# Kernel optimization log

Hardware: AMD Instinct MI355X
Metric: run time of the kernel (lower is better)

Reference implementation:

```python
import jax, jax.numpy as jnp
import numpy as np

NUM_Q_HEADS = 32
NUM_KV_HEADS = 8
HEAD_DIM = 128
ROPE_THETA = 10000.0


def _apply_rope(x, positions):
    # x: (B, T, H, D) real; rotate pairs (x[2i], x[2i+1]) by angle pos * inv_freq[i]
    B, T, H, D = x.shape
    half = D // 2
    inv_freq = 1.0 / (ROPE_THETA ** (jnp.arange(half, dtype=jnp.float32) / half))
    freqs = positions.astype(jnp.float32)[:, None] * inv_freq[None, :]  # (T, half)
    cos = jnp.cos(freqs)[None, :, None, :]  # (1, T, 1, half)
    sin = jnp.sin(freqs)[None, :, None, :]
    xr = x.reshape(B, T, H, half, 2)
    x1, x2 = xr[..., 0], xr[..., 1]
    o1 = x1 * cos - x2 * sin
    o2 = x1 * sin + x2 * cos
    return jnp.stack([o1, o2], axis=-1).reshape(B, T, H, D)


def setup_inputs() -> dict:
    key = jax.random.key(0)
    ks = jax.random.split(key, 8)
    B, T, C = 2, 1024, 4096
    x = jax.random.normal(ks[0], (B, T, C), dtype=jnp.float32)
    cache_keys = jax.random.normal(ks[1], (B, 4096, NUM_KV_HEADS, HEAD_DIM), dtype=jnp.float32)
    cache_values = jax.random.normal(ks[2], (B, 4096, NUM_KV_HEADS, HEAD_DIM), dtype=jnp.float32)
    s = 0.02
    Wq = jax.random.normal(ks[3], (C, C), dtype=jnp.float32) * s
    Wk = jax.random.normal(ks[4], (NUM_KV_HEADS * HEAD_DIM, C), dtype=jnp.float32) * s
    Wv = jax.random.normal(ks[5], (NUM_KV_HEADS * HEAD_DIM, C), dtype=jnp.float32) * s
    Wo = jax.random.normal(ks[6], (C, C), dtype=jnp.float32) * s
    return {"x": x, "start_pos": 1024, "cache_keys": cache_keys,
            "cache_values": cache_values, "Wq": Wq, "Wk": Wk, "Wv": Wv, "Wo": Wo}


def reference(x, start_pos, cache_keys, cache_values, Wq, Wk, Wv, Wo):
    B, T, C = x.shape
    D = HEAD_DIM
    G = NUM_Q_HEADS // NUM_KV_HEADS  # queries per kv head
    end_pos = start_pos + T
    scale = 1.0 / np.sqrt(D).astype(np.float32)

    # QKV projections (torch Linear: y = x @ W.T)
    q = jnp.einsum('btc,oc->bto', x, Wq).reshape(B, T, NUM_Q_HEADS, D)
    k = jnp.einsum('btc,oc->bto', x, Wk).reshape(B, T, NUM_KV_HEADS, D)
    v = jnp.einsum('btc,oc->bto', x, Wv).reshape(B, T, NUM_KV_HEADS, D)

    # RoPE at absolute positions [start_pos, end_pos)
    positions = jnp.arange(start_pos, end_pos)
    q = _apply_rope(q, positions)
    k = _apply_rope(k, positions)

    # KV-cache write (detached in the original -> stop_gradient)
    cache_keys = cache_keys.at[:, start_pos:end_pos].set(jax.lax.stop_gradient(k))
    cache_values = cache_values.at[:, start_pos:end_pos].set(jax.lax.stop_gradient(v))
    k_full = jax.lax.stop_gradient(cache_keys[:, :end_pos])   # (B, S, Hkv, D)
    v_full = jax.lax.stop_gradient(cache_values[:, :end_pos])
    S = end_pos

    # GQA attention without materializing repeated K/V:
    # q heads h map to kv head h // G (repeat_interleave ordering)
    qg = q.reshape(B, T, NUM_KV_HEADS, G, D)
    scores = jnp.einsum('btkgd,bskd->bkgts', qg, k_full) * scale  # (B,Hkv,G,T,S)

    # causal mask over the cache: query i sees cache positions j <= start_pos + i
    i = jnp.arange(T)[:, None]
    j = jnp.arange(S)[None, :]
    visible = j <= (start_pos + i)  # (T, S)
    scores = jnp.where(visible[None, None, None], scores, jnp.finfo(scores.dtype).min)
    probs = jax.nn.softmax(scores, axis=-1)

    ctx = jnp.einsum('bkgts,bskd->btkgd', probs, v_full).reshape(B, T, C)
    return jnp.einsum('btc,oc->bto', ctx, Wo)
```

## Files before the change

kernel.cpp:

```cpp
#include <hip/hip_runtime.h>
#include <math.h>


typedef __bf16 bf16x8 __attribute__((ext_vector_type(8)));
typedef float floatx4 __attribute__((ext_vector_type(4)));
typedef float floatx16 __attribute__((ext_vector_type(16)));

constexpr int SMAX = 2048;
constexpr size_t KT_OFF = (size_t)2 * 1024 * 4096;
constexpr size_t VT_OFF = KT_OFF + (size_t)2 * 8 * SMAX * 128;
constexpr size_t WS_XB = 0;
constexpr size_t WS_WQ = 8388608;
constexpr size_t WS_WK = 25165824;
constexpr size_t WS_WV = 29360128;
constexpr size_t WS_WO = 33554432;
constexpr size_t WS_FULL_BYTES = 100663296;

__device__ __forceinline__ unsigned short f2bf(float f) {
  union { float f; unsigned int u; } v; v.f = f;
  unsigned int u = v.u;
  return (unsigned short)((u + 0x7fffu + ((u >> 16) & 1u)) >> 16);
}

__device__ __forceinline__ bf16x8 pack8(float4 a, float4 b) {
  bf16x8 v;
  v[0] = (__bf16)a.x; v[1] = (__bf16)a.y; v[2] = (__bf16)a.z; v[3] = (__bf16)a.w;
  v[4] = (__bf16)b.x; v[5] = (__bf16)b.y; v[6] = (__bf16)b.z; v[7] = (__bf16)b.w;
  return v;
}

__device__ __forceinline__ unsigned cvtpk_bf16(float lo, float hi) {
  unsigned r;
  asm("v_cvt_pk_bf16_f32 %0, %1, %2" : "=v"(r) : "v"(lo), "v"(hi));
  return r;
}

__device__ __forceinline__ void gll16(const unsigned short* g, unsigned short* l) {
  __builtin_amdgcn_global_load_lds((const __attribute__((address_space(1))) void*)g,
                                   (__attribute__((address_space(3))) void*)l, 16, 0, 0);
}

__global__ __launch_bounds__(256) void cvt_x(const float* __restrict__ x,
                                             unsigned short* __restrict__ xb) {
  for (size_t c = (size_t)blockIdx.x * 256 + threadIdx.x; c < 1048576; c += (size_t)gridDim.x * 256) {
    float4 f0 = ((const float4*)x)[c * 2], f1 = ((const float4*)x)[c * 2 + 1];
    ((bf16x8*)xb)[c] = pack8(f0, f1);
  }
}

__global__ __launch_bounds__(256) void cvt_full(const float* __restrict__ x,
                                                const float* __restrict__ wq,
                                                const float* __restrict__ wk,
                                                const float* __restrict__ wv,
                                                const float* __restrict__ wo,
                                                unsigned short* __restrict__ ws) {
  const size_t n0 = 1048576, n1 = n0 + 2097152, n2 = n1 + 524288, n3 = n2 + 524288, n4 = n3 + 2097152;
  for (size_t c = (size_t)blockIdx.x * 256 + threadIdx.x; c < n4; c += (size_t)gridDim.x * 256) {
    const float* src; unsigned short* dst; size_t off;
    if (c < n0)      { src = x;  dst = ws + WS_XB; off = c; }
    else if (c < n1) { src = wq; dst = ws + WS_WQ; off = c - n0; }
    else if (c < n2) { src = wk; dst = ws + WS_WK; off = c - n1; }
    else if (c < n3) { src = wv; dst = ws + WS_WV; off = c - n2; }
    else             { src = wo; dst = ws + WS_WO; off = c - n3; }
    float4 f0 = ((const float4*)src)[off * 2], f1 = ((const float4*)src)[off * 2 + 1];
    ((bf16x8*)dst)[off] = pack8(f0, f1);
  }
}

__global__ __launch_bounds__(256) void rope_prep(const int* __restrict__ spp,
                                                 float* __restrict__ tab) {
  int idx = blockIdx.x * 256 + threadIdx.x;
  int t = idx >> 6, i = idx & 63;
  float ang = (float)(spp[0] + t) * exp2f(-(float)i * 0.2076205059304602f);
  tab[idx] = sinf(ang);
  tab[65536 + idx] = cosf(ang);
}

__global__ __launch_bounds__(256) void convert_cache(const float* __restrict__ ck,
                                                     const float* __restrict__ cv,
                                                     const int* __restrict__ spp,
                                                     unsigned short* __restrict__ kt,
                                                     unsigned short* __restrict__ vt) {
  const int sp = spp[0];
  const int bk = blockIdx.y;
  const int b = bk >> 3, kh = bk & 7;
  const int s1 = blockIdx.x * 128;
  if (s1 >= sp) return;
  const int tid = threadIdx.x;
#pragma unroll
  for (int it = 0; it < 8; ++it) {
    int c = tid + it * 256;
    int s = c >> 4, dc = (c & 15) * 8;
    if (s1 + s < sp) {
      const float* src = ck + (((size_t)(b * 4096 + s1 + s)) * 8 + kh) * 128 + dc;
      *(bf16x8*)(kt + ((size_t)bk * SMAX + s1 + s) * 128 + dc) = pack8(*(const float4*)src, *(const float4*)(src + 4));
    }
  }
#pragma unroll
  for (int it = 0; it < 8; ++it) {
    int c = tid + it * 256;
    int d = c & 127, sg = c >> 7;
    bf16x8 tmp;
#pragma unroll
    for (int ss = 0; ss < 8; ++ss) {
      int s = s1 + sg * 8 + ss;
      tmp[ss] = (s < sp) ? (__bf16)cv[(((size_t)(b * 4096 + s)) * 8 + kh) * 128 + d] : (__bf16)0.0f;
    }
    *(bf16x8*)(vt + (size_t)bk * 128 * SMAX + (size_t)d * SMAX + s1 + sg * 8) = tmp;
  }
}

template<bool BDMA, int EPI>
__global__ __launch_bounds__(256) void gemm_core(const unsigned short* __restrict__ A,
                                                 const unsigned short* __restrict__ Bb,
                                                 const float* __restrict__ Bq,
                                                 const float* __restrict__ Bk,
                                                 const float* __restrict__ Bv,
                                                 float* __restrict__ Cout,
                                                 unsigned short* __restrict__ qb,
                                                 unsigned short* __restrict__ kt,
                                                 unsigned short* __restrict__ vt,
                                                 const float* __restrict__ tab,
                                                 const int* __restrict__ spp) {
  constexpr int SB = BDMA ? 32 : 40;
  __shared__ __align__(16) unsigned short la[128 * 32];
  __shared__ __align__(16) unsigned short lb[128 * SB];
  const int K = 4096;
  const int tid = threadIdx.x, lane = tid & 63, wv = tid >> 6;
  const int quad = lane >> 4, l16 = lane & 15;
  const int wm = (wv >> 1) * 64, wn = (wv & 1) * 64;
  const int m0 = blockIdx.y * 128, n0 = blockIdx.x * 128;
  const int sp = spp ? spp[0] : 0;

  floatx4 acc[4][4] = {};

  const int r0 = tid >> 2, kc0 = (tid & 3) * 8;
  const int r1 = (tid + 256) >> 2, kc1 = ((tid + 256) & 3) * 8;
  const unsigned short* a0 = A + (size_t)(m0 + r0) * K + kc0;
  const unsigned short* a1 = A + (size_t)(m0 + r1) * K + kc1;

  const unsigned short* bh0 = nullptr; const unsigned short* bh1 = nullptr;
  const float* bf0 = nullptr; const float* bf1 = nullptr;
  if (BDMA) {
    bh0 = Bb + (size_t)(n0 + r0) * K + kc0;
    bh1 = Bb + (size_t)(n0 + r1) * K + kc1;
  } else {
    const float* Bf; int nb;
    if (EPI == 0)      { Bf = Bq; nb = n0; }
    else {
      if (n0 < 4096)      { Bf = Bq; nb = n0; }
      else if (n0 < 5120) { Bf = Bk; nb = n0 - 4096; }
      else                { Bf = Bv; nb = n0 - 5120; }
    }
    bf0 = Bf + (size_t)(nb + r0) * K + kc0;
    bf1 = Bf + (size_t)(nb + r1) * K + kc1;
  }

  for (int k0 = 0; k0 < K; k0 += 32) {
    gll16(a0 + k0, la + tid * 8);
    gll16(a1 + k0, la + (tid + 256) * 8);
    if (BDMA) {
      gll16(bh0 + k0, lb + tid * 8);
      gll16(bh1 + k0, lb + (tid + 256) * 8);
    } else {
      bf16x8 vb0 = pack8(*(const float4*)(bf0 + k0), *(const float4*)(bf0 + k0 + 4));
      bf16x8 vb1 = pack8(*(const float4*)(bf1 + k0), *(const float4*)(bf1 + k0 + 4));
      *(bf16x8*)(lb + r0 * 40 + kc0) = vb0;
      *(bf16x8*)(lb + r1 * 40 + kc1) = vb1;
    }
    __syncthreads();
    bf16x8 af[4], bfr[4];
#pragma unroll
    for (int mi = 0; mi < 4; ++mi)
      af[mi] = *(const bf16x8*)(la + (wm + mi * 16 + l16) * 32 + quad * 8);
#pragma unroll
    for (int ni = 0; ni < 4; ++ni)
      bfr[ni] = *(const bf16x8*)(lb + (wn + ni * 16 + l16) * SB + quad * 8);
#pragma unroll
    for (int mi = 0; mi < 4; ++mi)
#pragma unroll
      for (int ni = 0; ni < 4; ++ni)
        acc[mi][ni] = __builtin_amdgcn_mfma_f32_16x16x32_bf16(af[mi], bfr[ni], acc[mi][ni], 0, 0, 0);
    __syncthreads();
  }

  if (EPI == 0) {
#pragma unroll
    for (int mi = 0; mi < 4; ++mi)
#pragma unroll
      for (int r = 0; r < 4; ++r) {
        const int row = m0 + wm + mi * 16 + quad * 4 + r;
#pragma unroll
        for (int ni = 0; ni < 4; ++ni)
          Cout[(size_t)row * 4096 + n0 + wn + ni * 16 + l16] = acc[mi][ni][r];
      }
  } else {
    const float S_L2E = 0.12751745f;
#pragma unroll
    for (int mi = 0; mi < 4; ++mi) {
#pragma unroll
      for (int r = 0; r < 4; ++r) {
        const int row = m0 + wm + mi * 16 + quad * 4 + r;
        const int b = row >> 10, t = row & 1023;
#pragma unroll
        for (int ni = 0; ni < 4; ++ni) {
          const int col = n0 + wn + ni * 16 + l16;
          float v = acc[mi][ni][r];
          if (col < 5120) {
            int dd = col & 127, i = dd >> 1;
            float sn = tab[t * 64 + i], cs = tab[65536 + t * 64 + i];
            float vp = __shfl_xor(v, 1, 64);
            float o = (dd & 1) ? (vp * sn + v * cs) : (v * cs - vp * sn);
            if (col < 4096) {
              qb[(size_t)row * 4096 + col] = f2bf(o * S_L2E);
            } else {
              int lc = col - 4096, kh = lc >> 7, d = lc & 127;
              kt[((size_t)(b * 8 + kh) * SMAX + sp + t) * 128 + d] = f2bf(o);
            }
          } else {
            int lc = col - 5120, kh = lc >> 7, d = lc & 127;
            vt[((size_t)(b * 8 + kh) * 128 + d) * SMAX + sp + t] = f2bf(v);
          }
        }
      }
    }
  }
}

__global__ __launch_bounds__(512, 2) void attn(const unsigned short* __restrict__ qb,
                                               const unsigned short* __restrict__ ktg,
                                               const unsigned short* __restrict__ vtg,
                                               const int* __restrict__ spp,
                                               unsigned short* __restrict__ ctx) {
  __shared__ __align__(16) unsigned short lds[32768];

  const int sp = spp[0];
  const int iblk = (int)blockIdx.y * 4 + (int)blockIdx.x;
  const int lblk = (iblk & 7) * 32 + (iblk >> 3);
  const int x = lblk & 3, bh = lblk >> 2;
  const int b = bh >> 5, h = bh & 31;
  const int bk = b * 8 + (h >> 2);
  const int tid = threadIdx.x, lane = tid & 63, w = tid >> 6;
  const int hi = lane >> 5, l31 = lane & 31;
  const int tq128 = (w < 4) ? x : (7 - x);
  const int wq0 = tq128 * 128 + (w & 3) * 32;
  const int q = wq0 + l31;
  const int lim = sp + q;
  const int wlim = sp + wq0 + 31;
  const int nt = (sp + (8 - x) * 128 + 63) >> 6;

  const unsigned short* ktb = ktg + (size_t)bk * SMAX * 128;
  const unsigned short* vtb = vtg + (size_t)bk * 128 * SMAX;

  const int kr0 = tid >> 4, kc = tid & 15, kr1 = kr0 + 32;
  const int ksl0 = ((kc ^ (kr0 & 15)) << 3), ksl1 = ((kc ^ (kr1 & 15)) << 3);
  const int vd0 = tid >> 3, vc = tid & 7, vd1 = vd0 + 64;
  const int vsl0 = ((vc ^ (vd0 & 7)) << 3), vsl1 = ((vc ^ (vd1 & 7)) << 3);

  bf16x8 qf[8];
  {
    const unsigned short* qbase = qb + ((size_t)(b * 1024 + q)) * 4096 + h * 128 + hi * 8;
#pragma unroll
    for (int kg = 0; kg < 8; ++kg) qf[kg] = *(const bf16x8*)(qbase + kg * 16);
  }

  floatx16 oacc[4] = {};
  float mrun = -1e30f, lrun = 0.0f;

  *(bf16x8*)(lds + kr0 * 128 + ksl0)         = *(const bf16x8*)(ktb + (size_t)kr0 * 128 + kc * 8);
  *(bf16x8*)(lds + kr1 * 128 + ksl1)         = *(const bf16x8*)(ktb + (size_t)kr1 * 128 + kc * 8);
  *(bf16x8*)(lds + 16384 + vd0 * 64 + vsl0)  = *(const bf16x8*)(vtb + (size_t)vd0 * SMAX + vc * 8);
  *(bf16x8*)(lds + 16384 + vd1 * 64 + vsl1)  = *(const bf16x8*)(vtb + (size_t)vd1 * SMAX + vc * 8);
  __syncthreads();

  int off = 0;
  for (int st = 0; st < nt; ++st) {
    const int s0 = st * 64;
    bf16x8 nk0, nk1, nv0, nv1;
    const bool pre = (st + 1 < nt);
    if (pre) {
      const int s1 = s0 + 64;
      nk0 = *(const bf16x8*)(ktb + (size_t)(s1 + kr0) * 128 + kc * 8);
      nk1 = *(const bf16x8*)(ktb + (size_t)(s1 + kr1) * 128 + kc * 8);
      nv0 = *(const bf16x8*)(vtb + (size_t)vd0 * SMAX + s1 + vc * 8);
      nv1 = *(const bf16x8*)(vtb + (size_t)vd1 * SMAX + s1 + vc * 8);
      asm volatile("" ::: "memory");
    }
    const unsigned short* kl = lds + off;
    const unsigned short* vl = lds + 16384 + off;
    if (s0 <= wlim) {
#pragma unroll
      for (int sub = 0; sub < 2; ++sub) {
        const int ss = s0 + sub * 32;
        if (ss <= wlim) {
          floatx16 sa = {0,0,0,0,0,0,0,0,0,0,0,0,0,0,0,0};
          const unsigned short* kbase = kl + (sub * 32 + l31) * 128;
          const int kx = l31 & 15;
#pragma unroll
          for (int kg = 0; kg < 8; ++kg) {
            bf16x8 kf = *(const bf16x8*)(kbase + (((kg * 2 + hi) ^ kx) << 3));
            sa = __builtin_amdgcn_mfma_f32_32x32x16_bf16(kf, qf[kg], sa, 0, 0, 0);
          }
          if (ss + 31 > sp + wq0) {
#pragma unroll
            for (int r = 0; r < 16; ++r) {
              const int j = ss + (r & 3) + 8 * (r >> 2) + 4 * hi;
              if (j > lim) sa[r] = -1e30f;
            }
          }
          float mt = sa[0];
#pragma unroll
          for (int r = 1; r < 16; ++r) mt = fmaxf(mt, sa[r]);
          mt = fmaxf(mt, __shfl_xor(mt, 32, 64));
          if (!__all(mt <= mrun + 8.0f)) {
            const float mnew = fmaxf(mrun, mt);
            const float al = exp2f(mrun - mnew);
#pragma unroll
            for (int db = 0; db < 4; ++db)
#pragma unroll
              for (int r = 0; r < 16; ++r) oacc[db][r] *= al;
            lrun *= al;
            mrun = mnew;
          }
          float p[16]; float ls = 0.0f;
#pragma unroll
          for (int r = 0; r < 16; ++r) { p[r] = exp2f(sa[r] - mrun); ls += p[r]; }
          lrun += ls + __shfl_xor(ls, 32, 64);
#pragma unroll
          for (int ks = 0; ks < 2; ++ks) {
            const int rb = ks * 8;
            unsigned a0 = cvtpk_bf16(p[rb + 0], p[rb + 1]);
            unsigned a1 = cvtpk_bf16(p[rb + 2], p[rb + 3]);
            unsigned b0 = cvtpk_bf16(p[rb + 4], p[rb + 5]);
            unsigned b1 = cvtpk_bf16(p[rb + 6], p[rb + 7]);
            const unsigned t0 = __shfl_xor(a0, 32, 64);
            const unsigned t1 = __shfl_xor(b0, 32, 64);
            const unsigned t2 = __shfl_xor(a1, 32, 64);
            const unsigned t3 = __shfl_xor(b1, 32, 64);
            union { unsigned u[4]; bf16x8 v; } pf;
            pf.u[0] = hi ? t1 : a0;
            pf.u[1] = hi ? t3 : a1;
            pf.u[2] = hi ? b0 : t0;
            pf.u[3] = hi ? b1 : t2;
            const int sslot = sub * 4 + ks * 2 + hi;
#pragma unroll
            for (int db = 0; db < 4; ++db) {
              const int vrow = db * 32 + l31;
              bf16x8 vf = *(const bf16x8*)(vl + vrow * 64 + ((sslot ^ (l31 & 7)) << 3));
              oacc[db] = __builtin_amdgcn_mfma_f32_32x32x16_bf16(vf, pf.v, oacc[db], 0, 0, 0);
            }
          }
        }
      }
    }
    if (pre) {
      unsigned short* kn = lds + (off ^ 8192);
      unsigned short* vn = lds + 16384 + (off ^ 8192);
      *(bf16x8*)(kn + kr0 * 128 + ksl0) = nk0;
      *(bf16x8*)(kn + kr1 * 128 + ksl1) = nk1;
      *(bf16x8*)(vn + vd0 * 64 + vsl0) = nv0;
      *(bf16x8*)(vn + vd1 * 64 + vsl1) = nv1;
    }
    __syncthreads();
    off ^= 8192;
  }

  const float invl = 1.0f / lrun;
  unsigned short* myo = lds + w * 4096;
#pragma unroll
  for (int db = 0; db < 4; ++db)
#pragma unroll
    for (int i2 = 0; i2 < 8; ++i2) {
      const int r = i2 * 2;
      const int d = db * 32 + (r & 3) + 8 * (r >> 2) + 4 * hi;
      const unsigned wo = cvtpk_bf16(oacc[db][r] * invl, oacc[db][r + 1] * invl);
      *(unsigned*)(myo + l31 * 128 + (((2 * d) ^ ((l31 & 15) << 4)) >> 1)) = wo;
    }
  __syncthreads();
#pragma unroll
  for (int it = 0; it < 8; ++it) {
    const int c = tid + it * 512;
    const int wr = c >> 9, row = (c >> 4) & 31, c16 = c & 15;
    const int tq = (((wr < 4) ? x : (7 - x)) * 128) + (wr & 3) * 32 + row;
    bf16x8 vv = *(const bf16x8*)(lds + wr * 4096 + row * 128 + ((c16 ^ (row & 15)) << 3));
    *(bf16x8*)(ctx + ((size_t)(b * 1024 + tq)) * 4096 + h * 128 + c16 * 8) = vv;
  }
}

extern "C" void kernel_launch(void* const* d_in, const int* in_sizes, int n_in,
                              void* d_out, int out_size, void* d_ws, size_t ws_size,
                              hipStream_t stream) {
  const float* x  = (const float*)d_in[0];
  const int* sp   = (const int*)d_in[1];
  float* ck       = (float*)d_in[2];
  const float* cv = (const float*)d_in[3];
  const float* Wq = (const float*)d_in[4];
  const float* Wk = (const float*)d_in[5];
  const float* Wv = (const float*)d_in[6];
  const float* Wo = (const float*)d_in[7];
  float* out      = (float*)d_out;

  unsigned short* qb  = (unsigned short*)d_out;
  unsigned short* kt  = (unsigned short*)d_out + KT_OFF;
  unsigned short* vt  = (unsigned short*)d_out + VT_OFF;
  unsigned short* ws  = (unsigned short*)d_ws;
  unsigned short* xb  = ws + WS_XB;
  unsigned short* ctx = ws + WS_XB;
  float* tab          = ck + (size_t)2048 * 1024;

  const bool full = ws_size >= WS_FULL_BYTES;

  rope_prep<<<256, 256, 0, stream>>>(sp, tab);
  convert_cache<<<dim3(16, 16), 256, 0, stream>>>(ck, cv, sp, kt, vt);

  if (full) {
    cvt_full<<<2048, 256, 0, stream>>>(x, Wq, Wk, Wv, Wo, ws);
    gemm_core<true, 1><<<dim3(48, 16), 256, 0, stream>>>(xb, ws + WS_WQ, nullptr, nullptr, nullptr,
                                                         nullptr, qb, kt, vt, tab, sp);
    attn<<<dim3(4, 64), 512, 0, stream>>>(qb, kt, vt, sp, ctx);
    gemm_core<true, 0><<<dim3(32, 16), 256, 0, stream>>>(ctx, ws + WS_WO, nullptr, nullptr, nullptr,
                                                         out, nullptr, nullptr, nullptr, nullptr, nullptr);
  } else {
    cvt_x<<<2048, 256, 0, stream>>>(x, xb);
    gemm_core<false, 1><<<dim3(48, 16), 256, 0, stream>>>(xb, nullptr, Wq, Wk, Wv,
                                                          nullptr, qb, kt, vt, tab, sp);
    attn<<<dim3(4, 64), 512, 0, stream>>>(qb, kt, vt, sp, ctx);
    gemm_core<false, 0><<<dim3(32, 16), 256, 0, stream>>>(ctx, nullptr, Wo, nullptr, nullptr,
                                                          out, nullptr, nullptr, nullptr, nullptr, nullptr);
  }
}
```

Baseline: 593.2 us.

## Add 512-thread large-tile GEMM with 4-stage LDS pipeline for projections

Introduces a new gemm8 kernel with 256x256 (QKV) and 128x256 (output) tiles, 8 waves, a 4-deep global-to-LDS prefetch ring with explicit vmcnt waits, XOR-swizzled LDS slots, and a block-index remap so neighbouring workgroups share tiles. It replaces the older 128-wide gemm_core for both projections when the full workspace is available and the dynamic LDS attribute can be set. The aim is more data reuse per tile and better overlap of loads with MFMA work. In exchange it needs up to 128KB of LDS per block, which limits occupancy, and the hand-counted vmcnt values are fragile.

```diff
diff --git a/kernel.cpp b/kernel.cpp
--- a/kernel.cpp
+++ b/kernel.cpp
@@ -107,6 +107,154 @@
       tmp[ss] = (s < sp) ? (__bf16)cv[(((size_t)(b * 4096 + s)) * 8 + kh) * 128 + d] : (__bf16)0.0f;
     }
     *(bf16x8*)(vt + (size_t)bk * 128 * SMAX + (size_t)d * SMAX + s1 + sg * 8) = tmp;
+  }
+}
+
+template<int BM, int EPI>
+__global__ __launch_bounds__(512, 2) void gemm8(const unsigned short* __restrict__ A,
+                                                const unsigned short* __restrict__ B,
+                                                float* __restrict__ Cout,
+                                                unsigned short* __restrict__ qb,
+                                                unsigned short* __restrict__ kt,
+                                                unsigned short* __restrict__ vt,
+                                                const float* __restrict__ tab,
+                                                const int* __restrict__ spp) {
+  extern __shared__ unsigned short lds[];
+  constexpr int K = 4096;
+  constexpr int NT = K / 32;
+  constexpr int ASLOT = BM * 32;
+  constexpr int SLOT = ASLOT + 256 * 32;
+  constexpr int MI = (BM == 256) ? 8 : 4;
+  constexpr int NTN = (EPI == 1) ? 24 : 16;
+  constexpr int NWG = (EPI == 1) ? 192 : 256;
+
+  const int tid = threadIdx.x, lane = tid & 63, w = tid >> 6;
+  const int l16 = lane & 15, quad = lane >> 4;
+  const int wr = w >> 2, wc = w & 3;
+
+  const int bid = blockIdx.x;
+  const int lb = (bid & 7) * (NWG >> 3) + (bid >> 3);
+  const int mt = lb / NTN, nt = lb % NTN;
+  const int m0 = mt * BM, n0 = nt * 256;
+  const int sp = spp ? spp[0] : 0;
+
+  const int lrow = lane >> 2;
+  const int lslot = (lane & 3) ^ ((lane >> 3) & 3);
+  const unsigned short* ag = A + (size_t)(m0 + ((BM == 256) ? (w * 32) : (w * 16)) + lrow) * K + lslot * 8;
+  const unsigned short* bg = B + (size_t)(n0 + w * 32 + lrow) * K + lslot * 8;
+  const int adst0 = ((BM == 256) ? (w * 32) : (w * 16)) * 32;
+  const int bdst0 = ASLOT + (w * 32) * 32;
+
+  const int fslot = (quad ^ ((l16 >> 1) & 3)) * 8;
+  const int abase = ((BM == 256 ? wr * 128 : wr * 64) + l16) * 32 + fslot;
+  const int bbase = ASLOT + (wc * 64 + l16) * 32 + fslot;
+
+  floatx4 acc[MI][4] = {};
+
+  auto stage = [&](int t) {
+    unsigned short* sb = lds + (t & 3) * SLOT;
+    const int ko = t * 32;
+    gll16(ag + ko, sb + adst0);
+    if constexpr (BM == 256) gll16(ag + (size_t)16 * K + ko, sb + adst0 + 16 * 32);
+    gll16(bg + ko, sb + bdst0);
+    gll16(bg + (size_t)16 * K + ko, sb + bdst0 + 16 * 32);
+  };
+
+  auto compute = [&](int t) {
+    const unsigned short* sb = lds + (t & 3) * SLOT;
+    bf16x8 bfr[4];
+#pragma unroll
+    for (int ni = 0; ni < 4; ++ni)
+      bfr[ni] = *(const bf16x8*)(sb + bbase + ni * 512);
+    bf16x8 af[4];
+#pragma unroll
+    for (int mi = 0; mi < 4; ++mi)
+      af[mi] = *(const bf16x8*)(sb + abase + mi * 512);
+    __builtin_amdgcn_s_setprio(1);
+#pragma unroll
+    for (int mi = 0; mi < 4; ++mi)
+#pragma unroll
+      for (int ni = 0; ni < 4; ++ni)
+        acc[mi][ni] = __builtin_amdgcn_mfma_f32_16x16x32_bf16(af[mi], bfr[ni], acc[mi][ni], 0, 0, 0);
+    __builtin_amdgcn_s_setprio(0);
+    if constexpr (BM == 256) {
+      bf16x8 af2[4];
+#pragma unroll
+      for (int mi = 0; mi < 4; ++mi)
+        af2[mi] = *(const bf16x8*)(sb + abase + (mi + 4) * 512);
+      __builtin_amdgcn_s_setprio(1);
+#pragma unroll
+      for (int mi = 0; mi < 4; ++mi)
+#pragma unroll
+        for (int ni = 0; ni < 4; ++ni)
+          acc[mi + 4][ni] = __builtin_amdgcn_mfma_f32_16x16x32_bf16(af2[mi], bfr[ni], acc[mi + 4][ni], 0, 0, 0);
+      __builtin_amdgcn_s_setprio(0);
+    }
+  };
+
+  stage(0); stage(1); stage(2);
+  for (int t = 0; t < NT; ++t) {
+    if (t + 3 < NT) {
+      stage(t + 3);
+      if constexpr (BM == 256) asm volatile("s_waitcnt vmcnt(12)" ::: "memory");
+      else                     asm volatile("s_waitcnt vmcnt(9)" ::: "memory");
+    } else if (t + 3 == NT) {
+      if constexpr (BM == 256) asm volatile("s_waitcnt vmcnt(8)" ::: "memory");
+      else                     asm volatile("s_waitcnt vmcnt(6)" ::: "memory");
+    } else if (t + 2 == NT) {
+      if constexpr (BM == 256) asm volatile("s_waitcnt vmcnt(4)" ::: "memory");
+      else                     asm volatile("s_waitcnt vmcnt(3)" ::: "memory");
+    } else {
+      asm volatile("s_waitcnt vmcnt(0)" ::: "memory");
+    }
+    __builtin_amdgcn_s_barrier();
+    __builtin_amdgcn_sched_barrier(0);
+    compute(t);
+    asm volatile("s_waitcnt lgkmcnt(0)" ::: "memory");
+    __builtin_amdgcn_sched_barrier(0);
+    __builtin_amdgcn_s_barrier();
+  }
+
+  if constexpr (EPI == 0) {
+#pragma unroll
+    for (int mi = 0; mi < MI; ++mi)
+#pragma unroll
+      for (int r = 0; r < 4; ++r) {
+        const int row = m0 + wr * (BM / 2) + mi * 16 + quad * 4 + r;
+#pragma unroll
+        for (int ni = 0; ni < 4; ++ni)
+          Cout[(size_t)row * 4096 + n0 + wc * 64 + ni * 16 + l16] = acc[mi][ni][r];
+      }
+  } else {
+    const float S_L2E = 0.12751745f;
+#pragma unroll
+    for (int mi = 0; mi < MI; ++mi) {
+#pragma unroll
+      for (int r = 0; r < 4; ++r) {
+        const int row = m0 + wr * (BM / 2) + mi * 16 + quad * 4 + r;
+        const int bb = row >> 10, tt = row & 1023;
+#pragma unroll
+        for (int ni = 0; ni < 4; ++ni) {
+          const int col = n0 + wc * 64 + ni * 16 + l16;
+          float v = acc[mi][ni][r];
+          if (col < 5120) {
+            int dd = col & 127, i = dd >> 1;
+            float sn = tab[tt * 64 + i], cs = tab[65536 + tt * 64 + i];
+            float vp = __shfl_xor(v, 1, 64);
+            float o = (dd & 1) ? (vp * sn + v * cs) : (v * cs - vp * sn);
+            if (col < 4096) {
+              qb[(size_t)row * 4096 + col] = f2bf(o * S_L2E);
+            } else {
+              int lc = col - 4096, kh = lc >> 7, d = lc & 127;
+              kt[((size_t)(bb * 8 + kh) * SMAX + sp + tt) * 128 + d] = f2bf(o);
+            }
+          } else {
+            int lc = col - 5120, kh = lc >> 7, d = lc & 127;
+            vt[((size_t)(bb * 8 + kh) * 128 + d) * SMAX + sp + tt] = f2bf(v);
+          }
+        }
+      }
+    }
   }
 }
 
@@ -413,7 +561,21 @@
   rope_prep<<<256, 256, 0, stream>>>(sp, tab);
   convert_cache<<<dim3(16, 16), 256, 0, stream>>>(ck, cv, sp, kt, vt);
 
+  bool ok8 = false;
   if (full) {
+    ok8 = (hipFuncSetAttribute((const void*)gemm8<256, 1>,
+                               hipFuncAttributeMaxDynamicSharedMemorySize, 131072) == hipSuccess) &&
+          (hipFuncSetAttribute((const void*)gemm8<128, 0>,
+                               hipFuncAttributeMaxDynamicSharedMemorySize, 98304) == hipSuccess);
+  }
+
+  if (full && ok8) {
+    cvt_full<<<2048, 256, 0, stream>>>(x, Wq, Wk, Wv, Wo, ws);
+    gemm8<256, 1><<<192, 512, 131072, stream>>>(xb, ws + WS_WQ, nullptr, qb, kt, vt, tab, sp);
+    attn<<<dim3(4, 64), 512, 0, stream>>>(qb, kt, vt, sp, ctx);
+    gemm8<128, 0><<<256, 512, 98304, stream>>>(ctx, ws + WS_WO, out, nullptr, nullptr, nullptr,
+                                               nullptr, nullptr);
+  } else if (full) {
     cvt_full<<<2048, 256, 0, stream>>>(x, Wq, Wk, Wv, Wo, ws);
     gemm_core<true, 1><<<dim3(48, 16), 256, 0, stream>>>(xb, ws + WS_WQ, nullptr, nullptr, nullptr,
                                                          nullptr, qb, kt, vt, tab, sp);
```

Result: slower. 631.8 us (+6.5%).

## Add 4-stage direct-to-LDS pipelined GEMM with swizzled layout for projections

Applied to the files above, without the earlier changes.

Introduces a new bf16 GEMM kernel that replaces the previous gemm_core in the full-workspace path for both the fused QKV+RoPE projection and the output projection. It uses four LDS buffers with three tiles in flight via global-load-to-LDS, explicit vmcnt waits, an XOR-swizzled LDS layout to avoid bank conflicts, and raised wave priority around the MFMA block. The aim is to hide global memory latency and reduce barrier stalls in the K loop. The trade-off is more LDS per block (64KB), which may lower occupancy, plus reliance on hand-tuned waitcnt sequencing.

```diff
diff --git a/kernel.cpp b/kernel.cpp
--- a/kernel.cpp
+++ b/kernel.cpp
@@ -107,6 +107,115 @@
       tmp[ss] = (s < sp) ? (__bf16)cv[(((size_t)(b * 4096 + s)) * 8 + kh) * 128 + d] : (__bf16)0.0f;
     }
     *(bf16x8*)(vt + (size_t)bk * 128 * SMAX + (size_t)d * SMAX + s1 + sg * 8) = tmp;
+  }
+}
+
+template<int EPI>
+__global__ __launch_bounds__(256) void gemm_r2(const unsigned short* __restrict__ A,
+                                               const unsigned short* __restrict__ B,
+                                               float* __restrict__ Cout,
+                                               unsigned short* __restrict__ qb,
+                                               unsigned short* __restrict__ kt,
+                                               unsigned short* __restrict__ vt,
+                                               const float* __restrict__ tab,
+                                               const int* __restrict__ spp) {
+  __shared__ __align__(16) unsigned short lds[4 * 8192];
+  constexpr int K = 4096, NT = 128;
+  const int tid = threadIdx.x, lane = tid & 63, wv = tid >> 6;
+  const int quad = lane >> 4, l16 = lane & 15;
+  const int wm = (wv >> 1) * 64, wn = (wv & 1) * 64;
+  const int m0 = blockIdx.y * 128, n0 = blockIdx.x * 128;
+  const int sp = spp ? spp[0] : 0;
+
+  floatx4 acc[4][4] = {};
+
+  const int r0 = tid >> 2, r1 = r0 + 64;
+  const int sl = ((tid & 3) ^ ((tid >> 3) & 3)) * 8;
+  const unsigned short* a0 = A + (size_t)(m0 + r0) * K + sl;
+  const unsigned short* a1 = A + (size_t)(m0 + r1) * K + sl;
+  const unsigned short* b0 = B + (size_t)(n0 + r0) * K + sl;
+  const unsigned short* b1 = B + (size_t)(n0 + r1) * K + sl;
+  const int d0 = tid * 8, d1 = d0 + 2048;
+
+  const int fx = (quad ^ ((l16 >> 1) & 3)) * 8;
+  const int abase = (wm + l16) * 32 + fx;
+  const int bbase = 4096 + (wn + l16) * 32 + fx;
+
+  auto stage = [&](int t) {
+    unsigned short* sb = lds + (t & 3) * 8192;
+    const int ko = t * 32;
+    gll16(a0 + ko, sb + d0);
+    gll16(a1 + ko, sb + d1);
+    gll16(b0 + ko, sb + 4096 + d0);
+    gll16(b1 + ko, sb + 4096 + d1);
+  };
+
+  stage(0); stage(1); stage(2);
+  for (int t = 0; t < NT; ++t) {
+    if (t + 3 <= NT)      asm volatile("s_waitcnt vmcnt(8)" ::: "memory");
+    else if (t + 2 == NT) asm volatile("s_waitcnt vmcnt(4)" ::: "memory");
+    else                  asm volatile("s_waitcnt vmcnt(0)" ::: "memory");
+    __builtin_amdgcn_s_barrier();
+    __builtin_amdgcn_sched_barrier(0);
+    if (t + 3 < NT) stage(t + 3);
+    const unsigned short* sb = lds + (t & 3) * 8192;
+    bf16x8 af[4], bfr[4];
+#pragma unroll
+    for (int mi = 0; mi < 4; ++mi)
+      af[mi] = *(const bf16x8*)(sb + abase + mi * 512);
+#pragma unroll
+    for (int ni = 0; ni < 4; ++ni)
+      bfr[ni] = *(const bf16x8*)(sb + bbase + ni * 512);
+    __builtin_amdgcn_s_setprio(1);
+#pragma unroll
+    for (int mi = 0; mi < 4; ++mi)
+#pragma unroll
+      for (int ni = 0; ni < 4; ++ni)
+        acc[mi][ni] = __builtin_amdgcn_mfma_f32_16x16x32_bf16(af[mi], bfr[ni], acc[mi][ni], 0, 0, 0);
+    __builtin_amdgcn_s_setprio(0);
+    asm volatile("s_waitcnt lgkmcnt(0)" ::: "memory");
+  }
+
+  if constexpr (EPI == 0) {
+#pragma unroll
+    for (int mi = 0; mi < 4; ++mi)
+#pragma unroll
+      for (int r = 0; r < 4; ++r) {
+        const int row = m0 + wm + mi * 16 + quad * 4 + r;
+#pragma unroll
+        for (int ni = 0; ni < 4; ++ni)
+          Cout[(size_t)row * 4096 + n0 + wn + ni * 16 + l16] = acc[mi][ni][r];
+      }
+  } else {
+    const float S_L2E = 0.12751745f;
+#pragma unroll
+    for (int mi = 0; mi < 4; ++mi) {
+#pragma unroll
+      for (int r = 0; r < 4; ++r) {
+        const int row = m0 + wm + mi * 16 + quad * 4 + r;
+        const int bb = row >> 10, tt = row & 1023;
+#pragma unroll
+        for (int ni = 0; ni < 4; ++ni) {
+          const int col = n0 + wn + ni * 16 + l16;
+          float v = acc[mi][ni][r];
+          if (col < 5120) {
+            int dd = col & 127, i = dd >> 1;
+            float sn = tab[tt * 64 + i], cs = tab[65536 + tt * 64 + i];
+            float vp = __shfl_xor(v, 1, 64);
+            float o = (dd & 1) ? (vp * sn + v * cs) : (v * cs - vp * sn);
+            if (col < 4096) {
+              qb[(size_t)row * 4096 + col] = f2bf(o * S_L2E);
+            } else {
+              int lc = col - 4096, kh = lc >> 7, d = lc & 127;
+              kt[((size_t)(bb * 8 + kh) * SMAX + sp + tt) * 128 + d] = f2bf(o);
+            }
+          } else {
+            int lc = col - 5120, kh = lc >> 7, d = lc & 127;
+            vt[((size_t)(bb * 8 + kh) * 128 + d) * SMAX + sp + tt] = f2bf(v);
+          }
+        }
+      }
+    }
   }
 }
 
@@ -415,11 +524,10 @@
 
   if (full) {
     cvt_full<<<2048, 256, 0, stream>>>(x, Wq, Wk, Wv, Wo, ws);
-    gemm_core<true, 1><<<dim3(48, 16), 256, 0, stream>>>(xb, ws + WS_WQ, nullptr, nullptr, nullptr,
-                                                         nullptr, qb, kt, vt, tab, sp);
+    gemm_r2<1><<<dim3(48, 16), 256, 0, stream>>>(xb, ws + WS_WQ, nullptr, qb, kt, vt, tab, sp);
     attn<<<dim3(4, 64), 512, 0, stream>>>(qb, kt, vt, sp, ctx);
-    gemm_core<true, 0><<<dim3(32, 16), 256, 0, stream>>>(ctx, ws + WS_WO, nullptr, nullptr, nullptr,
-                                                         out, nullptr, nullptr, nullptr, nullptr, nullptr);
+    gemm_r2<0><<<dim3(32, 16), 256, 0, stream>>>(ctx, ws + WS_WO, out, nullptr, nullptr, nullptr,
+                                                 nullptr, nullptr);
   } else {
     cvt_x<<<2048, 256, 0, stream>>>(x, xb);
     gemm_core<false, 1><<<dim3(48, 16), 256, 0, stream>>>(xb, nullptr, Wq, Wk, Wv,
```

After: 609.9 us. +2.8%, slower.
